# Kernel tuning notes

Measured on AMD Instinct MI355X. Metric: run time of the kernel, lower is better.

Reference implementation:

```python
import jax, jax.numpy as jnp
import numpy as np

NUM_NODES = 262144
NUM_GRAPHS = 256
D_MODEL = 256
LOG_2 = float(np.log(2.0))


def setup_inputs() -> dict:
    key = jax.random.key(0)
    k1, k2, k3 = jax.random.split(key, 3)
    l_enc = jax.random.normal(k1, (NUM_NODES, D_MODEL), dtype=jnp.float32)
    g_enc = jax.random.normal(k2, (NUM_GRAPHS, D_MODEL), dtype=jnp.float32)
    batch = jax.random.randint(k3, (NUM_NODES,), 0, NUM_GRAPHS, dtype=jnp.int64)
    return {"l_enc": l_enc, "g_enc": g_enc, "batch": batch}


def reference(l_enc, g_enc, batch):
    # local_global_loss_ with measure='JSD', mask=[] (msk == ones)
    num_nodes = l_enc.shape[0]
    num_graphs = g_enc.shape[0]
    # pos_mask: one-hot of graph id per node; neg_mask is its complement
    pos_mask = jax.nn.one_hot(batch, num_graphs, dtype=l_enc.dtype)  # [N, G]
    neg_mask = 1.0 - pos_mask
    res = jnp.einsum('nd,gd->ng', l_enc, g_enc)                      # [N, G]
    # JSD positive expectation on res*pos_mask (zeros contribute 0)
    Ep = LOG_2 - jax.nn.softplus(-(res * pos_mask))
    # JSD negative expectation on res*neg_mask (zeros contribute 0)
    rq = res * neg_mask
    Eq = jax.nn.softplus(-rq) + rq - LOG_2
    E_pos = jnp.sum(Ep) / num_nodes
    E_neg = jnp.sum(Eq) / (num_nodes * (num_graphs - 1))
    return E_neg - E_pos
```

## Files before the change

kernel.cpp:

```cpp
#include <hip/hip_runtime.h>
#include <hip/hip_bf16.h>

#define N_NODES 262144
#define N_GRAPHS 256
#define DMODEL 256
#define LOG2_F 0.69314718055994530942f

typedef __attribute__((ext_vector_type(4))) float f32x4;
typedef __attribute__((ext_vector_type(8))) short short8;

__device__ __forceinline__ short bf(float x) {
    __hip_bfloat16 h = __float2bfloat16(x);
    return __builtin_bit_cast(short, h);
}

__device__ __forceinline__ short8 cvt8(f32x4 lo, f32x4 hi) {
    short8 a;
    a[0] = bf(lo[0]); a[1] = bf(lo[1]); a[2] = bf(lo[2]); a[3] = bf(lo[3]);
    a[4] = bf(hi[0]); a[5] = bf(hi[1]); a[6] = bf(hi[2]); a[7] = bf(hi[3]);
    return a;
}

__device__ __forceinline__ void mfma8(short8 a, const char* bb, f32x4* acc) {
#pragma unroll
    for (int nt = 0; nt < 8; ++nt) {
        short8 bfrag = *reinterpret_cast<const short8*>(bb + nt * 1024);
        acc[nt] = __builtin_amdgcn_mfma_f32_16x16x32_bf16(a, bfrag, acc[nt], 0, 0, 0);
    }
}

__global__ void pack_b_kernel(const float* __restrict__ g_enc,
                              short* __restrict__ bout) {
    int b = blockIdx.x;
    int lane = threadIdx.x;
    int ks = b >> 4, nt = b & 15;
    int g = nt * 16 + (lane & 15);
    int k = ks * 32 + (lane >> 4) * 8;
    const float* src = g_enc + g * DMODEL + k;
    short8 v;
#pragma unroll
    for (int j = 0; j < 8; ++j) v[j] = bf(src[j]);
    reinterpret_cast<short8*>(bout)[b * 64 + lane] = v;
}

__global__ __launch_bounds__(512, 1) void mvgrl_main(
    const float* __restrict__ l_enc, const int* __restrict__ batch,
    const short* __restrict__ bpack, double* __restrict__ partials) {
    extern __shared__ char lds_raw[];

    const int tid = threadIdx.x;
    const int lane = tid & 63;
    const int wave = tid >> 6;
    const int wrow = wave & 3;
    const int chalf = wave >> 2;

    {
        const short8* bp = reinterpret_cast<const short8*>(bpack);
        short8* lb = reinterpret_cast<short8*>(lds_raw);
#pragma unroll
        for (int c = 0; c < 16; ++c) {
            int chunk = wave + c * 8;
            lb[chunk * 64 + lane] = bp[chunk * 64 + lane];
        }
    }
    __syncthreads();

    const int row_blk = blockIdx.x * 1024;
    const char* ldsB = lds_raw + chalf * 8192 + lane * 16;
    double dSall = 0.0, dSpq = 0.0, dSpr = 0.0;

    f32x4 s0l, s0h, s1l, s1h, s2l, s2h, s3l, s3h;

    const float* arow = l_enc +
        (size_t)(row_blk + wrow * 16 + (lane & 15)) * DMODEL + (lane >> 4) * 8;
    s0l = *reinterpret_cast<const f32x4*>(arow + 0);
    s0h = *reinterpret_cast<const f32x4*>(arow + 4);
    s1l = *reinterpret_cast<const f32x4*>(arow + 32);
    s1h = *reinterpret_cast<const f32x4*>(arow + 36);
    s2l = *reinterpret_cast<const f32x4*>(arow + 64);
    s2h = *reinterpret_cast<const f32x4*>(arow + 68);
    s3l = *reinterpret_cast<const f32x4*>(arow + 96);
    s3h = *reinterpret_cast<const f32x4*>(arow + 100);

#pragma unroll 1
    for (int pass = 0; pass < 16; ++pass) {
        const int rowbase = row_blk + pass * 64 + wrow * 16;
        const int rsub = (lane >> 4) * 4;
        int bv0 = batch[rowbase + rsub + 0];
        int bv1 = batch[rowbase + rsub + 1];
        int bv2 = batch[rowbase + rsub + 2];
        int bv3 = batch[rowbase + rsub + 3];

        const float* arow_next = l_enc +
            (size_t)(row_blk + ((pass + 1) & 15) * 64 + wrow * 16 + (lane & 15)) *
                DMODEL + (lane >> 4) * 8;

        f32x4 acc[8];
#pragma unroll
        for (int n = 0; n < 8; ++n) acc[n] = (f32x4){0.f, 0.f, 0.f, 0.f};

#pragma unroll 1
        for (int g = 0; g < 2; ++g) {
            const float* src = (g == 0) ? (arow + 128) : arow_next;
            const char* lb = ldsB + (size_t)g * 4 * 16384;
            {
                short8 a = cvt8(s0l, s0h);
                s0l = *reinterpret_cast<const f32x4*>(src + 0);
                s0h = *reinterpret_cast<const f32x4*>(src + 4);
                mfma8(a, lb + 0 * 16384, acc);
            }
            {
                short8 a = cvt8(s1l, s1h);
                s1l = *reinterpret_cast<const f32x4*>(src + 32);
                s1h = *reinterpret_cast<const f32x4*>(src + 36);
                mfma8(a, lb + 1 * 16384, acc);
            }
            {
                short8 a = cvt8(s2l, s2h);
                s2l = *reinterpret_cast<const f32x4*>(src + 64);
                s2h = *reinterpret_cast<const f32x4*>(src + 68);
                mfma8(a, lb + 2 * 16384, acc);
            }
            {
                short8 a = cvt8(s3l, s3h);
                s3l = *reinterpret_cast<const f32x4*>(src + 96);
                s3h = *reinterpret_cast<const f32x4*>(src + 100);
                mfma8(a, lb + 3 * 16384, acc);
            }
        }
        arow = arow_next;

        float Sall = 0.f, Spq = 0.f, Spr = 0.f;
        const int colbase = chalf * 128 + (lane & 15);
#pragma unroll
        for (int nt = 0; nt < 8; ++nt) {
            const int col = colbase + nt * 16;
            f32x4 av = acc[nt];
            {
                float r = av[0];
                float q = fmaxf(r, 0.f) - LOG2_F + __logf(1.f + __expf(-fabsf(r)));
                Sall += q; if (col == bv0) { Spq += q; Spr += r; }
            }
            {
                float r = av[1];
                float q = fmaxf(r, 0.f) - LOG2_F + __logf(1.f + __expf(-fabsf(r)));
                Sall += q; if (col == bv1) { Spq += q; Spr += r; }
            }
            {
                float r = av[2];
                float q = fmaxf(r, 0.f) - LOG2_F + __logf(1.f + __expf(-fabsf(r)));
                Sall += q; if (col == bv2) { Spq += q; Spr += r; }
            }
            {
                float r = av[3];
                float q = fmaxf(r, 0.f) - LOG2_F + __logf(1.f + __expf(-fabsf(r)));
                Sall += q; if (col == bv3) { Spq += q; Spr += r; }
            }
        }
        dSall += (double)Sall;
        dSpq += (double)Spq;
        dSpr += (double)Spr;
    }

#pragma unroll
    for (int off = 32; off; off >>= 1) {
        dSall += __shfl_xor(dSall, off);
        dSpq += __shfl_xor(dSpq, off);
        dSpr += __shfl_xor(dSpr, off);
    }
    __syncthreads();
    double* red = reinterpret_cast<double*>(lds_raw);
    if (lane == 0) {
        red[wave * 3 + 0] = dSall;
        red[wave * 3 + 1] = dSpq;
        red[wave * 3 + 2] = dSpr;
    }
    __syncthreads();
    if (tid == 0) {
        double a = 0, b = 0, c = 0;
#pragma unroll
        for (int w = 0; w < 8; ++w) {
            a += red[w * 3 + 0];
            b += red[w * 3 + 1];
            c += red[w * 3 + 2];
        }
        partials[blockIdx.x * 3 + 0] = a;
        partials[blockIdx.x * 3 + 1] = b;
        partials[blockIdx.x * 3 + 2] = c;
    }
}

__global__ void finalize_kernel(const double* __restrict__ p,
                                float* __restrict__ out) {
    int t = threadIdx.x;
    double a = p[t * 3 + 0], b = p[t * 3 + 1], c = p[t * 3 + 2];
#pragma unroll
    for (int off = 32; off; off >>= 1) {
        a += __shfl_xor(a, off);
        b += __shfl_xor(b, off);
        c += __shfl_xor(c, off);
    }
    __shared__ double red[12];
    int lane = t & 63, w = t >> 6;
    if (lane == 0) { red[w * 3] = a; red[w * 3 + 1] = b; red[w * 3 + 2] = c; }
    __syncthreads();
    if (t == 0) {
        double A = 0, B = 0, C = 0;
#pragma unroll
        for (int i = 0; i < 4; ++i) {
            A += red[i * 3]; B += red[i * 3 + 1]; C += red[i * 3 + 2];
        }
        double neg = (A - B) / ((double)N_NODES * (double)(N_GRAPHS - 1));
        double pos = (C - B) / (double)N_NODES;
        out[0] = (float)(neg - pos);
    }
}

extern "C" void kernel_launch(void* const* d_in, const int* in_sizes, int n_in,
                              void* d_out, int out_size, void* d_ws,
                              size_t ws_size, hipStream_t stream) {
    const float* l_enc = (const float*)d_in[0];
    const float* g_enc = (const float*)d_in[1];
    const int* batch = (const int*)d_in[2];
    float* out = (float*)d_out;

    short* bpack = (short*)d_ws;
    double* partials = (double*)((char*)d_ws + 131072);

    hipFuncSetAttribute(reinterpret_cast<const void*>(mvgrl_main),
                        hipFuncAttributeMaxDynamicSharedMemorySize, 131072);

    pack_b_kernel<<<128, 64, 0, stream>>>(g_enc, bpack);
    mvgrl_main<<<256, 512, 131072, stream>>>(l_enc, batch, bpack, partials);
    finalize_kernel<<<1, 256, 0, stream>>>(partials, out);
}
```

Measured before the change: 90.04 us.

## Process two 16-row M tiles per wave to reuse each LDS B fragment

Each wave now computes two 16-row tiles (32 rows) per pass instead of one, so every B fragment read from LDS feeds two MFMAs. This halves LDS traffic per MFMA and the pass count drops from 16 to 8. The register prefetch pipeline is reorganised into even/odd k-chunk pairs, each covering both row tiles. In exchange, accumulator registers double to 16 f32x4, which raises register pressure, and the prefetch depth shrinks from four k-chunks to two per tile.

```diff
diff --git a/kernel.cpp b/kernel.cpp
--- a/kernel.cpp
+++ b/kernel.cpp
@@ -21,11 +21,13 @@
     return a;
 }
 
-__device__ __forceinline__ void mfma8(short8 a, const char* bb, f32x4* acc) {
+__device__ __forceinline__ void mfma16(short8 a0, short8 a1, const char* bb,
+                                       f32x4* accA, f32x4* accB) {
 #pragma unroll
     for (int nt = 0; nt < 8; ++nt) {
         short8 bfrag = *reinterpret_cast<const short8*>(bb + nt * 1024);
-        acc[nt] = __builtin_amdgcn_mfma_f32_16x16x32_bf16(a, bfrag, acc[nt], 0, 0, 0);
+        accA[nt] = __builtin_amdgcn_mfma_f32_16x16x32_bf16(a0, bfrag, accA[nt], 0, 0, 0);
+        accB[nt] = __builtin_amdgcn_mfma_f32_16x16x32_bf16(a1, bfrag, accB[nt], 0, 0, 0);
     }
 }
 
@@ -69,63 +71,66 @@
     const char* ldsB = lds_raw + chalf * 8192 + lane * 16;
     double dSall = 0.0, dSpq = 0.0, dSpr = 0.0;
 
-    f32x4 s0l, s0h, s1l, s1h, s2l, s2h, s3l, s3h;
-
+    f32x4 se0l, se0h, se1l, se1h, so0l, so0h, so1l, so1h;
+
+    const int kofs = (lane >> 4) * 8;
     const float* arow = l_enc +
-        (size_t)(row_blk + wrow * 16 + (lane & 15)) * DMODEL + (lane >> 4) * 8;
-    s0l = *reinterpret_cast<const f32x4*>(arow + 0);
-    s0h = *reinterpret_cast<const f32x4*>(arow + 4);
-    s1l = *reinterpret_cast<const f32x4*>(arow + 32);
-    s1h = *reinterpret_cast<const f32x4*>(arow + 36);
-    s2l = *reinterpret_cast<const f32x4*>(arow + 64);
-    s2h = *reinterpret_cast<const f32x4*>(arow + 68);
-    s3l = *reinterpret_cast<const f32x4*>(arow + 96);
-    s3h = *reinterpret_cast<const f32x4*>(arow + 100);
+        (size_t)(row_blk + wrow * 32 + (lane & 15)) * DMODEL + kofs;
+    const float* am1 = arow + 16 * DMODEL;
+    se0l = *reinterpret_cast<const f32x4*>(arow + 0);
+    se0h = *reinterpret_cast<const f32x4*>(arow + 4);
+    se1l = *reinterpret_cast<const f32x4*>(am1 + 0);
+    se1h = *reinterpret_cast<const f32x4*>(am1 + 4);
+    so0l = *reinterpret_cast<const f32x4*>(arow + 32);
+    so0h = *reinterpret_cast<const f32x4*>(arow + 36);
+    so1l = *reinterpret_cast<const f32x4*>(am1 + 32);
+    so1h = *reinterpret_cast<const f32x4*>(am1 + 36);
 
 #pragma unroll 1
-    for (int pass = 0; pass < 16; ++pass) {
-        const int rowbase = row_blk + pass * 64 + wrow * 16;
+    for (int pass = 0; pass < 8; ++pass) {
+        const int rowbase = row_blk + pass * 128 + wrow * 32;
         const int rsub = (lane >> 4) * 4;
-        int bv0 = batch[rowbase + rsub + 0];
-        int bv1 = batch[rowbase + rsub + 1];
-        int bv2 = batch[rowbase + rsub + 2];
-        int bv3 = batch[rowbase + rsub + 3];
+        int bvA0 = batch[rowbase + rsub + 0];
+        int bvA1 = batch[rowbase + rsub + 1];
+        int bvA2 = batch[rowbase + rsub + 2];
+        int bvA3 = batch[rowbase + rsub + 3];
+        int bvB0 = batch[rowbase + 16 + rsub + 0];
+        int bvB1 = batch[rowbase + 16 + rsub + 1];
+        int bvB2 = batch[rowbase + 16 + rsub + 2];
+        int bvB3 = batch[rowbase + 16 + rsub + 3];
 
         const float* arow_next = l_enc +
-            (size_t)(row_blk + ((pass + 1) & 15) * 64 + wrow * 16 + (lane & 15)) *
-                DMODEL + (lane >> 4) * 8;
-
-        f32x4 acc[8];
-#pragma unroll
-        for (int n = 0; n < 8; ++n) acc[n] = (f32x4){0.f, 0.f, 0.f, 0.f};
+            (size_t)(row_blk + ((pass + 1) & 7) * 128 + wrow * 32 + (lane & 15)) *
+                DMODEL + kofs;
+
+        f32x4 accA[8], accB[8];
+#pragma unroll
+        for (int n = 0; n < 8; ++n) {
+            accA[n] = (f32x4){0.f, 0.f, 0.f, 0.f};
+            accB[n] = (f32x4){0.f, 0.f, 0.f, 0.f};
+        }
 
 #pragma unroll 1
-        for (int g = 0; g < 2; ++g) {
-            const float* src = (g == 0) ? (arow + 128) : arow_next;
-            const char* lb = ldsB + (size_t)g * 4 * 16384;
-            {
-                short8 a = cvt8(s0l, s0h);
-                s0l = *reinterpret_cast<const f32x4*>(src + 0);
-                s0h = *reinterpret_cast<const f32x4*>(src + 4);
-                mfma8(a, lb + 0 * 16384, acc);
-            }
-            {
-                short8 a = cvt8(s1l, s1h);
-                s1l = *reinterpret_cast<const f32x4*>(src + 32);
-                s1h = *reinterpret_cast<const f32x4*>(src + 36);
-                mfma8(a, lb + 1 * 16384, acc);
-            }
-            {
-                short8 a = cvt8(s2l, s2h);
-                s2l = *reinterpret_cast<const f32x4*>(src + 64);
-                s2h = *reinterpret_cast<const f32x4*>(src + 68);
-                mfma8(a, lb + 2 * 16384, acc);
-            }
-            {
-                short8 a = cvt8(s3l, s3h);
-                s3l = *reinterpret_cast<const f32x4*>(src + 96);
-                s3h = *reinterpret_cast<const f32x4*>(src + 100);
-                mfma8(a, lb + 3 * 16384, acc);
+        for (int g = 0; g < 4; ++g) {
+            const float* srcE = (g < 3) ? (arow + (2 * g + 2) * 32) : arow_next;
+            const float* srcEm1 = srcE + 16 * DMODEL;
+            {
+                short8 a0 = cvt8(se0l, se0h);
+                short8 a1 = cvt8(se1l, se1h);
+                se0l = *reinterpret_cast<const f32x4*>(srcE + 0);
+                se0h = *reinterpret_cast<const f32x4*>(srcE + 4);
+                se1l = *reinterpret_cast<const f32x4*>(srcEm1 + 0);
+                se1h = *reinterpret_cast<const f32x4*>(srcEm1 + 4);
+                mfma16(a0, a1, ldsB + (size_t)(2 * g) * 16384, accA, accB);
+            }
+            {
+                short8 a0 = cvt8(so0l, so0h);
+                short8 a1 = cvt8(so1l, so1h);
+                so0l = *reinterpret_cast<const f32x4*>(srcE + 32);
+                so0h = *reinterpret_cast<const f32x4*>(srcE + 36);
+                so1l = *reinterpret_cast<const f32x4*>(srcEm1 + 32);
+                so1h = *reinterpret_cast<const f32x4*>(srcEm1 + 36);
+                mfma16(a0, a1, ldsB + (size_t)(2 * g + 1) * 16384, accA, accB);
             }
         }
         arow = arow_next;
@@ -135,26 +140,47 @@
 #pragma unroll
         for (int nt = 0; nt < 8; ++nt) {
             const int col = colbase + nt * 16;
-            f32x4 av = acc[nt];
-            {
-                float r = av[0];
-                float q = fmaxf(r, 0.f) - LOG2_F + __logf(1.f + __expf(-fabsf(r)));
-                Sall += q; if (col == bv0) { Spq += q; Spr += r; }
-            }
-            {
-                float r = av[1];
-                float q = fmaxf(r, 0.f) - LOG2_F + __logf(1.f + __expf(-fabsf(r)));
-                Sall += q; if (col == bv1) { Spq += q; Spr += r; }
-            }
-            {
-                float r = av[2];
-                float q = fmaxf(r, 0.f) - LOG2_F + __logf(1.f + __expf(-fabsf(r)));
-                Sall += q; if (col == bv2) { Spq += q; Spr += r; }
-            }
-            {
-                float r = av[3];
-                float q = fmaxf(r, 0.f) - LOG2_F + __logf(1.f + __expf(-fabsf(r)));
-                Sall += q; if (col == bv3) { Spq += q; Spr += r; }
+            f32x4 avA = accA[nt];
+            f32x4 avB = accB[nt];
+            {
+                float r = avA[0];
+                float q = fmaxf(r, 0.f) - LOG2_F + __logf(1.f + __expf(-fabsf(r)));
+                Sall += q; if (col == bvA0) { Spq += q; Spr += r; }
+            }
+            {
+                float r = avA[1];
+                float q = fmaxf(r, 0.f) - LOG2_F + __logf(1.f + __expf(-fabsf(r)));
+                Sall += q; if (col == bvA1) { Spq += q; Spr += r; }
+            }
+            {
+                float r = avA[2];
+                float q = fmaxf(r, 0.f) - LOG2_F + __logf(1.f + __expf(-fabsf(r)));
+                Sall += q; if (col == bvA2) { Spq += q; Spr += r; }
+            }
+            {
+                float r = avA[3];
+                float q = fmaxf(r, 0.f) - LOG2_F + __logf(1.f + __expf(-fabsf(r)));
+                Sall += q; if (col == bvA3) { Spq += q; Spr += r; }
+            }
+            {
+                float r = avB[0];
+                float q = fmaxf(r, 0.f) - LOG2_F + __logf(1.f + __expf(-fabsf(r)));
+                Sall += q; if (col == bvB0) { Spq += q; Spr += r; }
+            }
+            {
+                float r = avB[1];
+                float q = fmaxf(r, 0.f) - LOG2_F + __logf(1.f + __expf(-fabsf(r)));
+                Sall += q; if (col == bvB1) { Spq += q; Spr += r; }
+            }
+            {
+                float r = avB[2];
+                float q = fmaxf(r, 0.f) - LOG2_F + __logf(1.f + __expf(-fabsf(r)));
+                Sall += q; if (col == bvB2) { Spq += q; Spr += r; }
+            }
+            {
+                float r = avB[3];
+                float q = fmaxf(r, 0.f) - LOG2_F + __logf(1.f + __expf(-fabsf(r)));
+                Sall += q; if (col == bvB3) { Spq += q; Spr += r; }
             }
         }
         dSall += (double)Sall;
```

Result: no change. 91.84 us (+2.0%).
